# Kernel optimization log

Measured on AMD Instinct MI355X. Metric: run time of the kernel, lower is better.

Reference implementation:

```python
import jax, jax.numpy as jnp
import numpy as np

HEADS = 8
RANK = 4

def _lora(x, w_down, w_up, palette, in_dim, out_dim):
    # w_down: [RANK*in_dim, 15], w_up: [RANK*out_dim, 15], palette: [1, 15]
    down = (palette @ w_down.T).reshape(RANK, in_dim)   # [r, in]
    up = (palette @ w_up.T).reshape(out_dim, RANK)      # [out, r]
    return (x @ down.T) @ up.T                          # [..., out]


def setup_inputs() -> dict:
    key = jax.random.key(0)
    ks = jax.random.split(key, 16)
    B, S, D = 2, 2048, 1280
    def n(k, shape, std=0.02):
        return (jax.random.normal(k, shape, dtype=jnp.float32) * std).astype(jnp.float32)
    return {
        'hidden_states': jax.random.normal(ks[0], (B, S, D), dtype=jnp.float32),
        'color_palette': jax.random.uniform(ks[1], (1, 15), dtype=jnp.float32),
        'Wq': n(ks[2], (D, D)), 'Wk': n(ks[3], (D, D)),
        'Wv': n(ks[4], (D, D)), 'Wo': n(ks[5], (D, D)),
        'bo': jnp.zeros((D,), dtype=jnp.float32),
        'q_down': n(ks[6], (RANK * D, 15), 0.25), 'q_up': n(ks[7], (RANK * D, 15)),
        'k_down': n(ks[8], (RANK * D, 15), 0.25), 'k_up': n(ks[9], (RANK * D, 15)),
        'v_down': n(ks[10], (RANK * D, 15), 0.25), 'v_up': n(ks[11], (RANK * D, 15)),
        'o_down': n(ks[12], (RANK * D, 15), 0.25), 'o_up': n(ks[13], (RANK * D, 15)),
    }


def reference(hidden_states, color_palette, Wq, Wk, Wv, Wo, bo,
              q_down, q_up, k_down, k_up, v_down, v_up, o_down, o_up):
    B, S, D = hidden_states.shape
    H = HEADS
    hd = D // H
    scale = 1.0  # LoRA scale
    x = hidden_states
    # LoRA-augmented projections (self-attention: encoder_hidden_states = x)
    q = x @ Wq.T + scale * _lora(x, q_down, q_up, color_palette, D, D)
    k = x @ Wk.T + scale * _lora(x, k_down, k_up, color_palette, D, D)
    v = x @ Wv.T + scale * _lora(x, v_down, v_up, color_palette, D, D)
    # split heads: [B, S, D] -> [B, H, S, hd]
    q = q.reshape(B, S, H, hd).transpose(0, 2, 1, 3)
    k = k.reshape(B, S, H, hd).transpose(0, 2, 1, 3)
    v = v.reshape(B, S, H, hd).transpose(0, 2, 1, 3)
    attn_scale = 1.0 / jnp.sqrt(jnp.asarray(hd, dtype=q.dtype))
    scores = jnp.einsum('bhqd,bhkd->bhqk', q, k) * attn_scale
    probs = jax.nn.softmax(scores, axis=-1)
    out = jnp.einsum('bhqk,bhkd->bhqd', probs, v)
    out = out.transpose(0, 2, 1, 3).reshape(B, S, D)
    out = out @ Wo.T + bo + scale * _lora(out, o_down, o_up, color_palette, D, D)
    return out
```

## Files before the change

### kernel.cpp

```cpp
#include <hip/hip_runtime.h>

typedef unsigned short u16;
typedef unsigned int u32;
typedef __attribute__((ext_vector_type(4))) float floatx4;
typedef __attribute__((ext_vector_type(8))) __bf16 bf16x8;

#define MFMA_BF16(a, b, c) __builtin_amdgcn_mfma_f32_16x16x32_bf16((a), (b), (c), 0, 0, 0)

typedef const __attribute__((address_space(1))) void* gas_ptr;
typedef __attribute__((address_space(3))) void* las_ptr;

__device__ __forceinline__ void gll16(const void* g, void* l) {
  __builtin_amdgcn_global_load_lds((gas_ptr)g, (las_ptr)l, 16, 0, 0);
}

__device__ __forceinline__ u16 f2bf(float x) {
  u32 u = __builtin_bit_cast(u32, x);
  u = (u + 0x7fffu + ((u >> 16) & 1u)) >> 16;
  return (u16)u;
}

__global__ void prep_downup(const float* __restrict__ pal,
                            const float* __restrict__ qd, const float* __restrict__ qu,
                            const float* __restrict__ kd, const float* __restrict__ ku,
                            const float* __restrict__ vd, const float* __restrict__ vu,
                            const float* __restrict__ od, const float* __restrict__ ou,
                            float* __restrict__ down_f, float* __restrict__ up_f) {
  int tid = blockIdx.x * blockDim.x + threadIdx.x;
  int w = tid / 10240;
  int rem = tid - w * 10240;
  const float* dsrc = (w == 0) ? qd : (w == 1) ? kd : (w == 2) ? vd : od;
  const float* usrc = (w == 0) ? qu : (w == 1) ? ku : (w == 2) ? vu : ou;
  bool isdown = rem < 5120;
  int row = isdown ? rem : rem - 5120;
  const float* src = (isdown ? dsrc : usrc) + row * 15;
  float s = 0.f;
#pragma unroll
  for (int p = 0; p < 15; ++p) s += pal[p] * src[p];
  if (isdown) down_f[w * 5120 + row] = s;
  else        up_f[w * 5120 + row] = s;
}

__global__ void build_weff(const float* __restrict__ Wq, const float* __restrict__ Wk,
                           const float* __restrict__ Wv, const float* __restrict__ Wo,
                           const float* __restrict__ down_f, const float* __restrict__ up_f,
                           u16* __restrict__ weff_qkv, u16* __restrict__ weff_o) {
  int tid = blockIdx.x * blockDim.x + threadIdx.x;
  int w = tid / 1638400;
  int rem = tid - w * 1638400;
  int n = rem / 1280;
  int k = rem - n * 1280;
  const float* W = (w == 0) ? Wq : (w == 1) ? Wk : (w == 2) ? Wv : Wo;
  const float* up = up_f + w * 5120 + n * 4;
  const float* dn = down_f + w * 5120 + k;
  float v = W[rem] + up[0] * dn[0] + up[1] * dn[1280] + up[2] * dn[2560] + up[3] * dn[3840];
  u16 hv = f2bf(v);
  if (w < 3) weff_qkv[w * 1638400 + rem] = hv;
  else       weff_o[rem] = hv;
}

__global__ void cvt_x(const float4* __restrict__ x, ushort4* __restrict__ xb) {
  int i = blockIdx.x * blockDim.x + threadIdx.x;
  float4 v = x[i];
  ushort4 o;
  o.x = f2bf(v.x); o.y = f2bf(v.y); o.z = f2bf(v.z); o.w = f2bf(v.w);
  xb[i] = o;
}

__global__ __launch_bounds__(256) void gemm128_qkv(const u16* __restrict__ A, const u16* __restrict__ Bm,
                                                   u16* __restrict__ qb, u16* __restrict__ kb,
                                                   u16* __restrict__ vbuf, int K) {
  __shared__ __align__(16) u16 lA[128 * 64];
  __shared__ __align__(16) u16 lB[128 * 64];
  const int t = threadIdx.x;
  const int lane = t & 63;
  const int l15 = lane & 15, quad = lane >> 4;
  const int wid = t >> 6;
  const int wm = (wid >> 1) * 64;
  const int wn = (wid & 1) * 64;
  const int bm = blockIdx.x * 128;
  const int bn = blockIdx.y * 128;
  floatx4 acc[4][4] = {};

  int soff[4];
#pragma unroll
  for (int i = 0; i < 4; ++i) {
    int c = t + i * 256;
    int row = c >> 3, pos = c & 7;
    soff[i] = row * K + ((pos + row) & 7) * 8;
  }
  int afo[4][2], bfo[4][2];
#pragma unroll
  for (int i = 0; i < 4; ++i) {
#pragma unroll
    for (int ch = 0; ch < 2; ++ch) {
      int ra = wm + i * 16 + l15;
      int rb = wn + i * 16 + l15;
      int kc8 = ch * 4 + quad;
      afo[i][ch] = ra * 64 + ((kc8 - ra) & 7) * 8;
      bfo[i][ch] = rb * 64 + ((kc8 - rb) & 7) * 8;
    }
  }

  const u16* Ab = A + (long)bm * K;
  const u16* Bb = Bm + (long)bn * K;
  const int nkt = K >> 6;

  for (int kt = 0; kt < nkt; ++kt) {
    __syncthreads();
    const int k0 = kt * 64;
#pragma unroll
    for (int i = 0; i < 4; ++i) gll16(Ab + (long)soff[i] + k0, lA + (t + i * 256) * 8);
#pragma unroll
    for (int i = 0; i < 4; ++i) gll16(Bb + (long)soff[i] + k0, lB + (t + i * 256) * 8);
    __syncthreads();
#pragma unroll
    for (int ch = 0; ch < 2; ++ch) {
      bf16x8 af[4], bfr[4];
#pragma unroll
      for (int i = 0; i < 4; ++i) af[i] = *(const bf16x8*)(lA + afo[i][ch]);
#pragma unroll
      for (int i = 0; i < 4; ++i) bfr[i] = *(const bf16x8*)(lB + bfo[i][ch]);
#pragma unroll
      for (int i = 0; i < 4; ++i)
#pragma unroll
        for (int j = 0; j < 4; ++j)
          acc[i][j] = MFMA_BF16(af[i], bfr[j], acc[i][j]);
    }
  }

#pragma unroll
  for (int i = 0; i < 4; ++i) {
#pragma unroll
    for (int j = 0; j < 4; ++j) {
#pragma unroll
      for (int r = 0; r < 4; ++r) {
        int m = bm + wm + i * 16 + quad * 4 + r;
        int n = bn + wn + j * 16 + l15;
        u16 hv = f2bf(acc[i][j][r]);
        if (n < 1280) {
          qb[(long)m * 1280 + n] = hv;
        } else if (n < 2560) {
          kb[(long)m * 1280 + (n - 1280)] = hv;
        } else {
          vbuf[(long)m * 1280 + (n - 2560)] = hv;
        }
      }
    }
  }
}

__global__ __launch_bounds__(256) void vtrans(const u16* __restrict__ vbuf,
                                              u16* __restrict__ vtb) {
  __shared__ u16 tile[64 * 65];
  const int t = threadIdx.x;
  const int sb = blockIdx.x * 64, nb = blockIdx.y * 64, b = blockIdx.z;
  const u16* src = vbuf + ((long)(b * 2048 + sb)) * 1280 + nb;
#pragma unroll
  for (int it = 0; it < 16; ++it) {
    int idx = t + it * 256;
    int s = idx >> 6, n = idx & 63;
    tile[s * 65 + n] = src[(long)s * 1280 + n];
  }
  __syncthreads();
  u16* dst = vtb + ((long)(b * 1280 + nb)) * 2048 + sb;
#pragma unroll
  for (int it = 0; it < 16; ++it) {
    int idx = t + it * 256;
    int n = idx >> 6, s = idx & 63;
    dst[(long)n * 2048 + s] = tile[s * 65 + n];
  }
}

__global__ __launch_bounds__(256) void gemm64_o(const u16* __restrict__ A, const u16* __restrict__ Bm,
                                                float* __restrict__ outf,
                                                const float* __restrict__ bias, int K) {
  __shared__ __align__(16) u16 lA[64 * 64];
  __shared__ __align__(16) u16 lB[128 * 64];
  const int t = threadIdx.x;
  const int lane = t & 63;
  const int l15 = lane & 15, quad = lane >> 4;
  const int wid = t >> 6;
  const int bm = blockIdx.x * 64;
  const int bn = blockIdx.y * 128;
  floatx4 acc[4][2] = {};

  int aoff[2], boff[4];
#pragma unroll
  for (int i = 0; i < 2; ++i) {
    int c = t + i * 256;
    int row = c >> 3, pos = c & 7;
    aoff[i] = row * K + ((pos + row) & 7) * 8;
  }
#pragma unroll
  for (int i = 0; i < 4; ++i) {
    int c = t + i * 256;
    int row = c >> 3, pos = c & 7;
    boff[i] = row * K + ((pos + row) & 7) * 8;
  }
  int afo[4][2], bfo[2][2];
#pragma unroll
  for (int ch = 0; ch < 2; ++ch) {
    int kc8 = ch * 4 + quad;
#pragma unroll
    for (int i = 0; i < 4; ++i) {
      int ra = i * 16 + l15;
      afo[i][ch] = ra * 64 + ((kc8 - ra) & 7) * 8;
    }
#pragma unroll
    for (int j = 0; j < 2; ++j) {
      int rb = wid * 32 + j * 16 + l15;
      bfo[j][ch] = rb * 64 + ((kc8 - rb) & 7) * 8;
    }
  }

  const u16* Ab = A + (long)bm * K;
  const u16* Bb = Bm + (long)bn * K;
  const int nkt = K >> 6;

  for (int kt = 0; kt < nkt; ++kt) {
    __syncthreads();
    const int k0 = kt * 64;
#pragma unroll
    for (int i = 0; i < 2; ++i) gll16(Ab + (long)aoff[i] + k0, lA + (t + i * 256) * 8);
#pragma unroll
    for (int i = 0; i < 4; ++i) gll16(Bb + (long)boff[i] + k0, lB + (t + i * 256) * 8);
    __syncthreads();
#pragma unroll
    for (int ch = 0; ch < 2; ++ch) {
      bf16x8 af[4], bfr[2];
#pragma unroll
      for (int i = 0; i < 4; ++i) af[i] = *(const bf16x8*)(lA + afo[i][ch]);
#pragma unroll
      for (int j = 0; j < 2; ++j) bfr[j] = *(const bf16x8*)(lB + bfo[j][ch]);
#pragma unroll
      for (int i = 0; i < 4; ++i)
#pragma unroll
        for (int j = 0; j < 2; ++j)
          acc[i][j] = MFMA_BF16(af[i], bfr[j], acc[i][j]);
    }
  }

#pragma unroll
  for (int i = 0; i < 4; ++i) {
#pragma unroll
    for (int j = 0; j < 2; ++j) {
#pragma unroll
      for (int r = 0; r < 4; ++r) {
        int m = bm + i * 16 + quad * 4 + r;
        int n = bn + wid * 32 + j * 16 + l15;
        outf[(long)m * 1280 + n] = acc[i][j][r] + bias[n];
      }
    }
  }
}

__global__ __launch_bounds__(512) void flash_attn(const u16* __restrict__ qb,
                                                  const u16* __restrict__ kb,
                                                  const u16* __restrict__ vtb,
                                                  u16* __restrict__ attn) {
  const int S = 2048, D = 1280, HD = 160;
  __shared__ __align__(16) u16 kv_lds[2][64 * 160 + 160 * 64];
  __shared__ __align__(16) u16 p_lds[8][16 * 76];
  const int t = threadIdx.x, lane = t & 63, wid = t >> 6;
  const int quad = lane >> 4, l15 = lane & 15;
  const int bh = blockIdx.y, b = bh >> 3, h = bh & 7;
  const int q0 = blockIdx.x * 128 + wid * 16;
  const float kS = 0.11404582025f;

  bf16x8 aq[5];
  {
    const u16* qg = qb + ((long)(b * 2048 + q0 + l15)) * D + h * HD + quad * 8;
#pragma unroll
    for (int dc = 0; dc < 5; ++dc) aq[dc] = *(const bf16x8*)(qg + dc * 32);
  }

  const u16* sg[5];
  int sadv[5];
#pragma unroll
  for (int i = 0; i < 5; ++i) {
    int c = t + i * 512;
    if (c < 1280) {
      int key = c / 20, pos = c - key * 20;
      int ccol = pos - (key % 20);
      if (ccol < 0) ccol += 20;
      sg[i] = kb + ((long)(b * 2048 + key)) * D + h * HD + ccol * 8;
      sadv[i] = 64 * D;
    } else {
      int c2 = c - 1280;
      int vrow = c2 >> 3, swz = c2 & 7;
      int vcol = swz ^ (vrow & 7);
      sg[i] = vtb + ((long)(b * 1280 + h * HD + vrow)) * 2048 + vcol * 8;
      sadv[i] = 64;
    }
  }

  int kfo[4][5];
#pragma unroll
  for (int j = 0; j < 4; ++j) {
    int key = j * 16 + l15;
    int r0 = (quad + key) % 20;
#pragma unroll
    for (int dc = 0; dc < 5; ++dc) {
      int rot = r0 + dc * 4;
      if (rot >= 20) rot -= 20;
      kfo[j][dc] = (key * 20 + rot) * 8;
    }
  }
  int vfo[10][2];
#pragma unroll
  for (int dc = 0; dc < 10; ++dc) {
    int row = dc * 16 + l15;
#pragma unroll
    for (int ks = 0; ks < 2; ++ks) {
      int sw = (ks * 4 + quad) ^ (row & 7);
      vfo[dc][ks] = 10240 + (row * 8 + sw) * 8;
    }
  }

  float l_part[4] = {0.f, 0.f, 0.f, 0.f};
  floatx4 o_acc[10] = {};

#pragma unroll
  for (int i = 0; i < 5; ++i) {
    gll16(sg[i], &kv_lds[0][0] + (t + i * 512) * 8);
    sg[i] += sadv[i];
  }

  for (int kt0 = 0; kt0 < 32; ++kt0) {
    u16* cbase = &kv_lds[kt0 & 1][0];
    if (kt0 < 31) {
      u16* nbase = &kv_lds[(kt0 & 1) ^ 1][0];
#pragma unroll
      for (int i = 0; i < 5; ++i) {
        gll16(sg[i], nbase + (t + i * 512) * 8);
        sg[i] += sadv[i];
      }
      asm volatile("s_waitcnt vmcnt(5)" ::: "memory");
    } else {
      asm volatile("s_waitcnt vmcnt(0)" ::: "memory");
    }
    __builtin_amdgcn_s_barrier();
    __builtin_amdgcn_sched_barrier(0);

    floatx4 s[4] = {};
#pragma unroll
    for (int dc = 0; dc < 5; ++dc) {
#pragma unroll
      for (int j = 0; j < 4; ++j) {
        bf16x8 kf = *(const bf16x8*)(cbase + kfo[j][dc]);
        s[j] = MFMA_BF16(aq[dc], kf, s[j]);
      }
    }

#pragma unroll
    for (int r = 0; r < 4; ++r) {
      float p0 = __builtin_exp2f(fminf(s[0][r] * kS, 80.f));
      float p1 = __builtin_exp2f(fminf(s[1][r] * kS, 80.f));
      float p2 = __builtin_exp2f(fminf(s[2][r] * kS, 80.f));
      float p3 = __builtin_exp2f(fminf(s[3][r] * kS, 80.f));
      l_part[r] += (p0 + p1) + (p2 + p3);
      u16* pw = p_lds[wid] + (quad * 4 + r) * 76 + l15;
      pw[0]  = f2bf(p0);
      pw[16] = f2bf(p1);
      pw[32] = f2bf(p2);
      pw[48] = f2bf(p3);
    }
    asm volatile("s_waitcnt lgkmcnt(0)" ::: "memory");

    bf16x8 paA = *(const bf16x8*)(p_lds[wid] + l15 * 76 + quad * 8);
    bf16x8 paB = *(const bf16x8*)(p_lds[wid] + l15 * 76 + 32 + quad * 8);
#pragma unroll
    for (int dc = 0; dc < 10; ++dc) {
      bf16x8 vfA = *(const bf16x8*)(cbase + vfo[dc][0]);
      bf16x8 vfB = *(const bf16x8*)(cbase + vfo[dc][1]);
      o_acc[dc] = MFMA_BF16(paA, vfA, o_acc[dc]);
      o_acc[dc] = MFMA_BF16(paB, vfB, o_acc[dc]);
    }
    __builtin_amdgcn_sched_barrier(0);
    __builtin_amdgcn_s_barrier();
  }

  float rl[4];
#pragma unroll
  for (int r = 0; r < 4; ++r) {
    float rs = l_part[r];
    rs += __shfl_xor(rs, 1, 64);
    rs += __shfl_xor(rs, 2, 64);
    rs += __shfl_xor(rs, 4, 64);
    rs += __shfl_xor(rs, 8, 64);
    rl[r] = 1.0f / rs;
  }
#pragma unroll
  for (int dc = 0; dc < 10; ++dc) {
#pragma unroll
    for (int r = 0; r < 4; ++r) {
      float v = o_acc[dc][r] * rl[r];
      int row = q0 + quad * 4 + r;
      int col = h * HD + dc * 16 + l15;
      attn[((long)(b * 2048 + row)) * D + col] = f2bf(v);
    }
  }
}

extern "C" void kernel_launch(void* const* d_in, const int* in_sizes, int n_in,
                              void* d_out, int out_size, void* d_ws, size_t ws_size,
                              hipStream_t stream) {
  const float* x   = (const float*)d_in[0];
  const float* pal = (const float*)d_in[1];
  const float* Wq  = (const float*)d_in[2];
  const float* Wk  = (const float*)d_in[3];
  const float* Wv  = (const float*)d_in[4];
  const float* Wo  = (const float*)d_in[5];
  const float* bo  = (const float*)d_in[6];
  const float* qd  = (const float*)d_in[7];
  const float* qu  = (const float*)d_in[8];
  const float* kd  = (const float*)d_in[9];
  const float* ku  = (const float*)d_in[10];
  const float* vd  = (const float*)d_in[11];
  const float* vu  = (const float*)d_in[12];
  const float* od  = (const float*)d_in[13];
  const float* ou  = (const float*)d_in[14];
  float* out = (float*)d_out;

  char* ws = (char*)d_ws;
  u16* xb       = (u16*)(ws);
  u16* weff_qkv = (u16*)(ws + 10485760);
  u16* weff_o   = (u16*)(ws + 20316160);
  u16* qbuf     = (u16*)(ws + 23592960);
  u16* kbuf     = (u16*)(ws + 34078720);
  u16* vtb      = (u16*)(ws + 44564480);
  u16* attn     = (u16*)(ws + 55050240);
  float* down_f = (float*)(ws + 65536000);
  float* up_f   = (float*)(ws + 65617920);
  u16* vbuf     = (u16*)(ws + 65699840);

  prep_downup<<<160, 256, 0, stream>>>(pal, qd, qu, kd, ku, vd, vu, od, ou, down_f, up_f);
  build_weff<<<25600, 256, 0, stream>>>(Wq, Wk, Wv, Wo, down_f, up_f, weff_qkv, weff_o);
  cvt_x<<<5120, 256, 0, stream>>>((const float4*)x, (ushort4*)xb);
  gemm128_qkv<<<dim3(32, 30), 256, 0, stream>>>(xb, weff_qkv, qbuf, kbuf, vbuf, 1280);
  vtrans<<<dim3(32, 20, 2), 256, 0, stream>>>(vbuf, vtb);
  flash_attn<<<dim3(16, 16), 512, 0, stream>>>(qbuf, kbuf, vtb, attn);
  gemm64_o<<<dim3(64, 10), 256, 0, stream>>>(attn, weff_o, out, bo, 1280);
}
```

Before: 303.7 us.

## Switch flash attention to 32x32 MFMA with key-split wave pairs

```diff
diff --git a/kernel.cpp b/kernel.cpp
--- a/kernel.cpp
+++ b/kernel.cpp
@@ -3,9 +3,11 @@
 typedef unsigned short u16;
 typedef unsigned int u32;
 typedef __attribute__((ext_vector_type(4))) float floatx4;
+typedef __attribute__((ext_vector_type(16))) float floatx16;
 typedef __attribute__((ext_vector_type(8))) __bf16 bf16x8;
 
 #define MFMA_BF16(a, b, c) __builtin_amdgcn_mfma_f32_16x16x32_bf16((a), (b), (c), 0, 0, 0)
+#define MFMA32(a, b, c) __builtin_amdgcn_mfma_f32_32x32x16_bf16((a), (b), (c), 0, 0, 0)
 
 typedef const __attribute__((address_space(1))) void* gas_ptr;
 typedef __attribute__((address_space(3))) void* las_ptr;
@@ -259,20 +261,21 @@
                                                   const u16* __restrict__ kb,
                                                   const u16* __restrict__ vtb,
                                                   u16* __restrict__ attn) {
-  const int S = 2048, D = 1280, HD = 160;
-  __shared__ __align__(16) u16 kv_lds[2][64 * 160 + 160 * 64];
-  __shared__ __align__(16) u16 p_lds[8][16 * 76];
+  const int D = 1280, HD = 160;
+  __shared__ __align__(16) u16 kv_lds[2][20480];
+  __shared__ __align__(16) u16 p_lds[8][1024];
   const int t = threadIdx.x, lane = t & 63, wid = t >> 6;
-  const int quad = lane >> 4, l15 = lane & 15;
+  const int l31 = lane & 31, hi = lane >> 5;
+  const int rg = wid >> 1, kh = wid & 1;
   const int bh = blockIdx.y, b = bh >> 3, h = bh & 7;
-  const int q0 = blockIdx.x * 128 + wid * 16;
+  const int q0 = blockIdx.x * 128 + rg * 32;
   const float kS = 0.11404582025f;
 
-  bf16x8 aq[5];
+  bf16x8 aq[10];
   {
-    const u16* qg = qb + ((long)(b * 2048 + q0 + l15)) * D + h * HD + quad * 8;
-#pragma unroll
-    for (int dc = 0; dc < 5; ++dc) aq[dc] = *(const bf16x8*)(qg + dc * 32);
+    const u16* qg = qb + ((long)(b * 2048 + q0 + l31)) * D + h * HD + hi * 8;
+#pragma unroll
+    for (int kw = 0; kw < 10; ++kw) aq[kw] = *(const bf16x8*)(qg + kw * 16);
   }
 
   const u16* sg[5];
@@ -295,31 +298,34 @@
     }
   }
 
-  int kfo[4][5];
-#pragma unroll
-  for (int j = 0; j < 4; ++j) {
-    int key = j * 16 + l15;
-    int r0 = (quad + key) % 20;
-#pragma unroll
-    for (int dc = 0; dc < 5; ++dc) {
-      int rot = r0 + dc * 4;
-      if (rot >= 20) rot -= 20;
-      kfo[j][dc] = (key * 20 + rot) * 8;
-    }
-  }
-  int vfo[10][2];
-#pragma unroll
-  for (int dc = 0; dc < 10; ++dc) {
-    int row = dc * 16 + l15;
-#pragma unroll
-    for (int ks = 0; ks < 2; ++ks) {
-      int sw = (ks * 4 + quad) ^ (row & 7);
-      vfo[dc][ks] = 10240 + (row * 8 + sw) * 8;
-    }
-  }
-
-  float l_part[4] = {0.f, 0.f, 0.f, 0.f};
-  floatx4 o_acc[10] = {};
+  int kfo[10];
+  {
+    int key = kh * 32 + l31;
+#pragma unroll
+    for (int kw = 0; kw < 10; ++kw) {
+      int g = kw * 2 + hi;
+      int pos = (g + key) % 20;
+      kfo[kw] = (key * 20 + pos) * 8;
+    }
+  }
+  int vfo[5][2];
+#pragma unroll
+  for (int db = 0; db < 5; ++db) {
+#pragma unroll
+    for (int kwv = 0; kwv < 2; ++kwv) {
+      int d = db * 32 + l31;
+      int gc = kh * 4 + kwv * 2 + hi;
+      int sw = gc ^ (d & 7);
+      vfo[db][kwv] = 10240 + (d * 8 + sw) * 8;
+    }
+  }
+  int pfo[2];
+#pragma unroll
+  for (int ks = 0; ks < 2; ++ks)
+    pfo[ks] = l31 * 64 + (((ks * 2 + hi) ^ (l31 & 3)) << 4);
+
+  float l_acc[16] = {};
+  floatx16 o_acc[5] = {};
 
 #pragma unroll
   for (int i = 0; i < 5; ++i) {
@@ -343,62 +349,75 @@
     __builtin_amdgcn_s_barrier();
     __builtin_amdgcn_sched_barrier(0);
 
-    floatx4 s[4] = {};
-#pragma unroll
-    for (int dc = 0; dc < 5; ++dc) {
-#pragma unroll
-      for (int j = 0; j < 4; ++j) {
-        bf16x8 kf = *(const bf16x8*)(cbase + kfo[j][dc]);
-        s[j] = MFMA_BF16(aq[dc], kf, s[j]);
-      }
-    }
-
-#pragma unroll
-    for (int r = 0; r < 4; ++r) {
-      float p0 = __builtin_exp2f(fminf(s[0][r] * kS, 80.f));
-      float p1 = __builtin_exp2f(fminf(s[1][r] * kS, 80.f));
-      float p2 = __builtin_exp2f(fminf(s[2][r] * kS, 80.f));
-      float p3 = __builtin_exp2f(fminf(s[3][r] * kS, 80.f));
-      l_part[r] += (p0 + p1) + (p2 + p3);
-      u16* pw = p_lds[wid] + (quad * 4 + r) * 76 + l15;
-      pw[0]  = f2bf(p0);
-      pw[16] = f2bf(p1);
-      pw[32] = f2bf(p2);
-      pw[48] = f2bf(p3);
+    floatx16 s0 = {}, s1 = {};
+#pragma unroll
+    for (int kw = 0; kw < 5; ++kw) {
+      bf16x8 k0 = *(const bf16x8*)(cbase + kfo[kw * 2]);
+      bf16x8 k1 = *(const bf16x8*)(cbase + kfo[kw * 2 + 1]);
+      s0 = MFMA32(aq[kw * 2], k0, s0);
+      s1 = MFMA32(aq[kw * 2 + 1], k1, s1);
+    }
+
+    u16* pw = p_lds[wid];
+#pragma unroll
+    for (int r = 0; r < 16; ++r) {
+      float sv = (s0[r] + s1[r]) * kS;
+      float p = __builtin_exp2f(fminf(sv, 80.f));
+      l_acc[r] += p;
+      int qr = (r & 3) + 8 * (r >> 2) + 4 * hi;
+      int boff = qr * 64 + (((l31 >> 3) ^ (r & 3)) << 4) + (l31 & 7) * 2;
+      *(u16*)((char*)pw + boff) = f2bf(p);
     }
     asm volatile("s_waitcnt lgkmcnt(0)" ::: "memory");
-
-    bf16x8 paA = *(const bf16x8*)(p_lds[wid] + l15 * 76 + quad * 8);
-    bf16x8 paB = *(const bf16x8*)(p_lds[wid] + l15 * 76 + 32 + quad * 8);
-#pragma unroll
-    for (int dc = 0; dc < 10; ++dc) {
-      bf16x8 vfA = *(const bf16x8*)(cbase + vfo[dc][0]);
-      bf16x8 vfB = *(const bf16x8*)(cbase + vfo[dc][1]);
-      o_acc[dc] = MFMA_BF16(paA, vfA, o_acc[dc]);
-      o_acc[dc] = MFMA_BF16(paB, vfB, o_acc[dc]);
+    __builtin_amdgcn_sched_barrier(0);
+
+    bf16x8 pa0 = *(const bf16x8*)((const char*)pw + pfo[0]);
+    bf16x8 pa1 = *(const bf16x8*)((const char*)pw + pfo[1]);
+#pragma unroll
+    for (int db = 0; db < 5; ++db) {
+      bf16x8 v0 = *(const bf16x8*)(cbase + vfo[db][0]);
+      bf16x8 v1 = *(const bf16x8*)(cbase + vfo[db][1]);
+      o_acc[db] = MFMA32(pa0, v0, o_acc[db]);
+      o_acc[db] = MFMA32(pa1, v1, o_acc[db]);
     }
     __builtin_amdgcn_sched_barrier(0);
     __builtin_amdgcn_s_barrier();
   }
 
-  float rl[4];
-#pragma unroll
-  for (int r = 0; r < 4; ++r) {
-    float rs = l_part[r];
-    rs += __shfl_xor(rs, 1, 64);
-    rs += __shfl_xor(rs, 2, 64);
-    rs += __shfl_xor(rs, 4, 64);
-    rs += __shfl_xor(rs, 8, 64);
-    rl[r] = 1.0f / rs;
-  }
-#pragma unroll
-  for (int dc = 0; dc < 10; ++dc) {
-#pragma unroll
-    for (int r = 0; r < 4; ++r) {
-      float v = o_acc[dc][r] * rl[r];
-      int row = q0 + quad * 4 + r;
-      int col = h * HD + dc * 16 + l15;
-      attn[((long)(b * 2048 + row)) * D + col] = f2bf(v);
+  float* oscr = (float*)&kv_lds[0][0];
+  float* lscr = (float*)&p_lds[0][0];
+  if (kh == 1) {
+#pragma unroll
+    for (int db = 0; db < 5; ++db)
+#pragma unroll
+      for (int r = 0; r < 16; ++r)
+        oscr[rg * 5120 + (db * 16 + r) * 64 + lane] = o_acc[db][r];
+#pragma unroll
+    for (int r = 0; r < 16; ++r)
+      lscr[rg * 1024 + r * 64 + lane] = l_acc[r];
+  }
+  __syncthreads();
+  if (kh == 0) {
+    float rl[16];
+#pragma unroll
+    for (int r = 0; r < 16; ++r) {
+      float rs = l_acc[r] + lscr[rg * 1024 + r * 64 + lane];
+      rs += __shfl_xor(rs, 1, 64);
+      rs += __shfl_xor(rs, 2, 64);
+      rs += __shfl_xor(rs, 4, 64);
+      rs += __shfl_xor(rs, 8, 64);
+      rs += __shfl_xor(rs, 16, 64);
+      rl[r] = 1.0f / rs;
+    }
+#pragma unroll
+    for (int db = 0; db < 5; ++db) {
+#pragma unroll
+      for (int r = 0; r < 16; ++r) {
+        float v = (o_acc[db][r] + oscr[rg * 5120 + (db * 16 + r) * 64 + lane]) * rl[r];
+        int row = q0 + (r & 3) + 8 * (r >> 2) + 4 * hi;
+        int col = h * HD + db * 32 + l31;
+        attn[((long)(b * 2048 + row)) * D + col] = f2bf(v);
+      }
     }
   }
 }
```

New measurement: 284.6 us. 1.07x faster.
